# Optimization experiments

Hardware: AMD Instinct MI355X
Metric: run time of the kernel (lower is better)

## Reference

```python
import jax, jax.numpy as jnp
import numpy as np

NUM_STEPS = 5  # DVF2DDF(num_steps=5)


def _warp(vol, ddf, mode):
    """MONAI Warp: sample vol at (voxel index + ddf), align_corners=True, zeros padding.
    vol: [N,C,D,H,W]; ddf: [N,3,D,H,W] (channels = d,h,w displacement)."""
    N, C, D, H, W = vol.shape
    gd, gh, gw = jnp.meshgrid(jnp.arange(D, dtype=ddf.dtype),
                              jnp.arange(H, dtype=ddf.dtype),
                              jnp.arange(W, dtype=ddf.dtype), indexing='ij')
    cd = gd + ddf[:, 0]  # [N,D,H,W] absolute sample coords
    ch = gh + ddf[:, 1]
    cw = gw + ddf[:, 2]
    vol_flat = vol.reshape(N, C, D * H * W)

    def gather(di, hi, wi, valid):
        dc = jnp.clip(di, 0, D - 1)
        hc = jnp.clip(hi, 0, H - 1)
        wc = jnp.clip(wi, 0, W - 1)
        flat = ((dc * H + hc) * W + wc).reshape(N, 1, -1)
        v = jnp.take_along_axis(vol_flat, flat, axis=2).reshape(N, C, D, H, W)
        return v * valid[:, None]

    def in_bounds(di, hi, wi):
        return ((di >= 0) & (di < D) & (hi >= 0) & (hi < H)
                & (wi >= 0) & (wi < W)).astype(vol.dtype)

    if mode == 'nearest':
        di = jnp.round(cd).astype(jnp.int32)
        hi = jnp.round(ch).astype(jnp.int32)
        wi = jnp.round(cw).astype(jnp.int32)
        return gather(di, hi, wi, in_bounds(di, hi, wi))

    # trilinear ('bilinear' in grid_sample naming)
    d0 = jnp.floor(cd); h0 = jnp.floor(ch); w0 = jnp.floor(cw)
    fd = cd - d0; fh = ch - h0; fw = cw - w0
    d0i = d0.astype(jnp.int32); h0i = h0.astype(jnp.int32); w0i = w0.astype(jnp.int32)
    out = jnp.zeros_like(vol)
    for dd in (0, 1):
        for dh in (0, 1):
            for dw in (0, 1):
                di = d0i + dd; hi = h0i + dh; wi = w0i + dw
                wgt = ((fd if dd else 1 - fd)
                       * (fh if dh else 1 - fh)
                       * (fw if dw else 1 - fw))
                out = out + gather(di, hi, wi, in_bounds(di, hi, wi)) * wgt[:, None]
    return out


def _dvf2ddf(dvf, num_steps=NUM_STEPS):
    """Scaling-and-squaring integration of a stationary velocity field (MONAI DVF2DDF)."""
    ddf = dvf / (2 ** num_steps)
    for _ in range(num_steps):
        ddf = ddf + _warp(ddf, ddf, 'bilinear')
    return ddf


def setup_inputs() -> dict:
    key = jax.random.key(0)
    ks = jax.random.split(key, 6)
    D = H = W = 160
    return {
        "dvf0": jax.random.normal(ks[0], (1, 3, D, H, W), jnp.float32),
        "dvf1": jax.random.normal(ks[1], (1, 3, D, H, W), jnp.float32),
        "image": jax.random.normal(ks[2], (1, 1, D, H, W), jnp.float32),
        "cavity": jax.random.randint(ks[3], (1, 1, D, H, W), 0, 5, jnp.int32),
        "coronary": jax.random.randint(ks[4], (1, 1, D, H, W), 0, 3, jnp.int32),
        "w": jax.random.uniform(ks[5], (), jnp.float32),
    }


def reference(dvf0, dvf1, image, cavity, coronary, w):
    # linear blend of the two neighbouring phase DVFs
    dvf = dvf0 * (1 - w) + dvf1 * w
    ddf = _dvf2ddf(dvf)
    img_warped = _warp(image, ddf, 'bilinear')
    # labels are concatenated along batch and warped with nearest, ddf repeated
    labels = jnp.concatenate([cavity, coronary], axis=0).astype(jnp.float32)  # [2,1,D,H,W]
    lab_warped = _warp(labels, jnp.tile(ddf, (2, 1, 1, 1, 1)), 'nearest')
    cav_warped = lab_warped[0][None].astype(jnp.uint8)
    cor_warped = lab_warped[1][None].astype(jnp.uint8)
    return img_warped, cav_warped, cor_warped, ddf
```

## Files before the change

### kernel.cpp

```cpp
#include <hip/hip_runtime.h>

#define DD 160
#define HH 160
#define WW 160
#define PL (HH*WW)
#define S (DD*PL)

__device__ __forceinline__ float fmul(float a, float b){ return __fmul_rn(a,b); }
__device__ __forceinline__ float fadd(float a, float b){ return __fadd_rn(a,b); }
__device__ __forceinline__ float fsub(float a, float b){ return __fsub_rn(a,b); }


template<int H>
__global__ __launch_bounds__(256) void warp_step(const float* __restrict__ in,
                                                 float* __restrict__ out) {
    constexpr int RX = 32 + 2 * H;
    constexpr int RY = 8 + 2 * H;
    constexpr int RZ = 4 + 2 * H;
    constexpr int CH = RX * RY * RZ;
    __shared__ float smem[3 * CH];

    int b  = (blockIdx.x & 7) * 500 + (blockIdx.x >> 3);
    int ix = b % 5;
    int r  = b / 5;
    int iy = r % 20;
    int iz = r / 20;
    int x0 = ix << 5, y0 = iy << 3, z0 = iz << 2;
    int xs = x0 - H, ys = y0 - H, zs = z0 - H;

    int tid = threadIdx.x;
    for (int s = tid; s < CH; s += 256) {
        int rz  = s / (RY * RX);
        int rem = s - rz * (RY * RX);
        int ry  = rem / RX;
        int rx  = rem - ry * RX;
        int cz = min(max(zs + rz, 0), DD - 1);
        int cy = min(max(ys + ry, 0), HH - 1);
        int cx = min(max(xs + rx, 0), WW - 1);
        int q = (cz * HH + cy) * WW + cx;
        smem[s]          = in[q];
        smem[CH + s]     = in[S + q];
        smem[2 * CH + s] = in[2 * S + q];
    }
    __syncthreads();

    int lane = tid & 63, wid = tid >> 6;
    int x = x0 | (lane & 31);
    int y = y0 | (wid << 1) | (lane >> 5);

    for (int j = 0; j < 4; ++j) {
        int z = z0 + j;
        int p = (z * HH + y) * WW + x;
        int lc = ((j + H) * RY + (y - ys)) * RX + (x - xs);
        float vd = smem[lc], vh = smem[CH + lc], vw = smem[2 * CH + lc];

        float cd = fadd((float)z, vd);
        float ch = fadd((float)y, vh);
        float cw = fadd((float)x, vw);

        float d0 = floorf(cd), h0 = floorf(ch), w0 = floorf(cw);
        float fd = fsub(cd, d0), fh = fsub(ch, h0), fw = fsub(cw, w0);
        float gd = fsub(1.0f, fd), gh = fsub(1.0f, fh), gw = fsub(1.0f, fw);
        int d0i = (int)d0, h0i = (int)h0, w0i = (int)w0;

        int rd = d0i - zs, rh = h0i - ys, rw = w0i - xs;
        bool ok = ((unsigned)rd < (unsigned)(RZ - 1))
                & ((unsigned)rh < (unsigned)(RY - 1))
                & ((unsigned)rw < (unsigned)(RX - 1));

        float r0, r1, r2;
        if (ok) {
            bool vA0 = (d0i >= 0), vA1 = (d0i + 1 < DD);
            bool vB0 = (h0i >= 0), vB1 = (h0i + 1 < HH);
            bool vC0 = (w0i >= 0), vC1 = (w0i + 1 < WW);
            float wt[8];
            #pragma unroll
            for (int t = 0; t < 8; ++t) {
                int dd = t >> 2, dh = (t >> 1) & 1, dw = t & 1;
                bool valid = (dd ? vA1 : vA0) & (dh ? vB1 : vB0) & (dw ? vC1 : vC0);
                float wgt = fmul(fmul(dd ? fd : gd, dh ? fh : gh), dw ? fw : gw);
                wt[t] = valid ? wgt : 0.0f;
            }
            int l0 = (rd * RY + rh) * RX + rw;
            const int off[8] = { 0, 1, RX, RX + 1,
                                 RY * RX, RY * RX + 1, (RY + 1) * RX, (RY + 1) * RX + 1 };
            float acc0 = 0.0f, acc1 = 0.0f, acc2 = 0.0f;
            #pragma unroll
            for (int t = 0; t < 8; ++t) {
                int li = l0 + off[t];
                acc0 = fadd(acc0, fmul(smem[li], wt[t]));
                acc1 = fadd(acc1, fmul(smem[CH + li], wt[t]));
                acc2 = fadd(acc2, fmul(smem[2 * CH + li], wt[t]));
            }
            r0 = fadd(vd, acc0);
            r1 = fadd(vh, acc1);
            r2 = fadd(vw, acc2);
        } else {
            int   qa[8];
            float wt[8];
            #pragma unroll
            for (int t = 0; t < 8; ++t) {
                int dd = t >> 2, dh = (t >> 1) & 1, dw = t & 1;
                int di = d0i + dd, hi = h0i + dh, wi = w0i + dw;
                bool valid = (di >= 0) & (di < DD) & (hi >= 0) & (hi < HH)
                           & (wi >= 0) & (wi < WW);
                float wgt = fmul(fmul(dd ? fd : gd, dh ? fh : gh), dw ? fw : gw);
                wt[t] = valid ? wgt : 0.0f;
                int dc = min(max(di, 0), DD - 1);
                int hc = min(max(hi, 0), HH - 1);
                int wc = min(max(wi, 0), WW - 1);
                qa[t] = (dc * HH + hc) * WW + wc;
            }
            float acc0 = 0.0f, acc1 = 0.0f, acc2 = 0.0f;
            #pragma unroll
            for (int t = 0; t < 8; ++t) {
                acc0 = fadd(acc0, fmul(in[qa[t]], wt[t]));
                acc1 = fadd(acc1, fmul(in[S + qa[t]], wt[t]));
                acc2 = fadd(acc2, fmul(in[2 * S + qa[t]], wt[t]));
            }
            r0 = fadd(vd, acc0);
            r1 = fadd(vh, acc1);
            r2 = fadd(vw, acc2);
        }

        out[p] = r0; out[S + p] = r1; out[2 * S + p] = r2;
    }
}

__global__ __launch_bounds__(256) void fused_init_s1(const float* __restrict__ dvf0,
                                                     const float* __restrict__ dvf1,
                                                     const float* __restrict__ wp,
                                                     float* __restrict__ out) {
    constexpr int H = 1, RX = 34, RY = 10, RZ = 6, CH = RX * RY * RZ;
    __shared__ float smem[3 * CH];
    float w = wp[0];
    float onew = fsub(1.0f, w);

    int b  = (blockIdx.x & 7) * 500 + (blockIdx.x >> 3);
    int ix = b % 5;
    int r  = b / 5;
    int iy = r % 20;
    int iz = r / 20;
    int x0 = ix << 5, y0 = iy << 3, z0 = iz << 2;
    int xs = x0 - H, ys = y0 - H, zs = z0 - H;

    int tid = threadIdx.x;
    for (int s = tid; s < CH; s += 256) {
        int rz  = s / (RY * RX);
        int rem = s - rz * (RY * RX);
        int ry  = rem / RX;
        int rx  = rem - ry * RX;
        int cz = min(max(zs + rz, 0), DD - 1);
        int cy = min(max(ys + ry, 0), HH - 1);
        int cx = min(max(xs + rx, 0), WW - 1);
        int q = (cz * HH + cy) * WW + cx;
        #pragma unroll
        for (int c = 0; c < 3; ++c) {
            float a = dvf0[(size_t)c * S + q];
            float bb = dvf1[(size_t)c * S + q];
            smem[c * CH + s] = fmul(fadd(fmul(a, onew), fmul(bb, w)), 0.03125f);
        }
    }
    __syncthreads();

    int lane = tid & 63, wid = tid >> 6;
    int x = x0 | (lane & 31);
    int y = y0 | (wid << 1) | (lane >> 5);

    for (int j = 0; j < 4; ++j) {
        int z = z0 + j;
        int p = (z * HH + y) * WW + x;
        int lc = ((j + H) * RY + (y - ys)) * RX + (x - xs);
        float vd = smem[lc], vh = smem[CH + lc], vw = smem[2 * CH + lc];

        float cd = fadd((float)z, vd);
        float ch = fadd((float)y, vh);
        float cw = fadd((float)x, vw);

        float d0 = floorf(cd), h0 = floorf(ch), w0 = floorf(cw);
        float fd = fsub(cd, d0), fh = fsub(ch, h0), fw = fsub(cw, w0);
        float gd = fsub(1.0f, fd), gh = fsub(1.0f, fh), gw = fsub(1.0f, fw);
        int d0i = (int)d0, h0i = (int)h0, w0i = (int)w0;

        int rd = d0i - zs, rh = h0i - ys, rw = w0i - xs;
        bool ok = ((unsigned)rd < (unsigned)(RZ - 1))
                & ((unsigned)rh < (unsigned)(RY - 1))
                & ((unsigned)rw < (unsigned)(RX - 1));

        float r0, r1, r2;
        if (ok) {
            bool vA0 = (d0i >= 0), vA1 = (d0i + 1 < DD);
            bool vB0 = (h0i >= 0), vB1 = (h0i + 1 < HH);
            bool vC0 = (w0i >= 0), vC1 = (w0i + 1 < WW);
            float wt[8];
            #pragma unroll
            for (int t = 0; t < 8; ++t) {
                int dd = t >> 2, dh = (t >> 1) & 1, dw = t & 1;
                bool valid = (dd ? vA1 : vA0) & (dh ? vB1 : vB0) & (dw ? vC1 : vC0);
                float wgt = fmul(fmul(dd ? fd : gd, dh ? fh : gh), dw ? fw : gw);
                wt[t] = valid ? wgt : 0.0f;
            }
            int l0 = (rd * RY + rh) * RX + rw;
            const int off[8] = { 0, 1, RX, RX + 1,
                                 RY * RX, RY * RX + 1, (RY + 1) * RX, (RY + 1) * RX + 1 };
            float acc0 = 0.0f, acc1 = 0.0f, acc2 = 0.0f;
            #pragma unroll
            for (int t = 0; t < 8; ++t) {
                int li = l0 + off[t];
                acc0 = fadd(acc0, fmul(smem[li], wt[t]));
                acc1 = fadd(acc1, fmul(smem[CH + li], wt[t]));
                acc2 = fadd(acc2, fmul(smem[2 * CH + li], wt[t]));
            }
            r0 = fadd(vd, acc0);
            r1 = fadd(vh, acc1);
            r2 = fadd(vw, acc2);
        } else {
            int   qa[8];
            float wt[8];
            #pragma unroll
            for (int t = 0; t < 8; ++t) {
                int dd = t >> 2, dh = (t >> 1) & 1, dw = t & 1;
                int di = d0i + dd, hi = h0i + dh, wi = w0i + dw;
                bool valid = (di >= 0) & (di < DD) & (hi >= 0) & (hi < HH)
                           & (wi >= 0) & (wi < WW);
                float wgt = fmul(fmul(dd ? fd : gd, dh ? fh : gh), dw ? fw : gw);
                wt[t] = valid ? wgt : 0.0f;
                int dc = min(max(di, 0), DD - 1);
                int hc = min(max(hi, 0), HH - 1);
                int wc = min(max(wi, 0), WW - 1);
                qa[t] = (dc * HH + hc) * WW + wc;
            }
            float acc0 = 0.0f, acc1 = 0.0f, acc2 = 0.0f;
            #pragma unroll
            for (int t = 0; t < 8; ++t) {
                float ga = fmul(fadd(fmul(dvf0[qa[t]], onew), fmul(dvf1[qa[t]], w)), 0.03125f);
                float gb = fmul(fadd(fmul(dvf0[S + qa[t]], onew), fmul(dvf1[S + qa[t]], w)), 0.03125f);
                float gc = fmul(fadd(fmul(dvf0[2 * S + qa[t]], onew), fmul(dvf1[2 * S + qa[t]], w)), 0.03125f);
                acc0 = fadd(acc0, fmul(ga, wt[t]));
                acc1 = fadd(acc1, fmul(gb, wt[t]));
                acc2 = fadd(acc2, fmul(gc, wt[t]));
            }
            r0 = fadd(vd, acc0);
            r1 = fadd(vh, acc1);
            r2 = fadd(vw, acc2);
        }

        out[p] = r0; out[S + p] = r1; out[2 * S + p] = r2;
    }
}

__global__ __launch_bounds__(256) void final_fused(const float* __restrict__ ddf4,
                                                   const float* __restrict__ image,
                                                   const int* __restrict__ cav,
                                                   const int* __restrict__ cor,
                                                   float* __restrict__ outImg,
                                                   float* __restrict__ outDdf) {
    int b  = (blockIdx.x & 7) * 1000 + (blockIdx.x >> 3);
    int ix = b % 5;
    int r  = b / 5;
    int iy = r % 20;
    int iz = r / 20;
    int lane = threadIdx.x & 63, wid = threadIdx.x >> 6;
    int x  = (ix << 5) | (lane & 31);
    int y  = (iy << 3) | (wid << 1) | (lane >> 5);
    int z0 = iz << 1;
    int p0 = (z0 * HH + y) * WW + x;

    #pragma unroll
    for (int j = 0; j < 2; ++j) {
        int z = z0 + j;
        int p = p0 + j * PL;

        float vd = ddf4[p], vh = ddf4[S + p], vw = ddf4[2 * S + p];
        float cd = fadd((float)z, vd);
        float ch = fadd((float)y, vh);
        float cw = fadd((float)x, vw);

        float d0 = floorf(cd), h0 = floorf(ch), w0 = floorf(cw);
        float fd = fsub(cd, d0), fh = fsub(ch, h0), fw = fsub(cw, w0);
        float gd = fsub(1.0f, fd), gh = fsub(1.0f, fh), gw = fsub(1.0f, fw);
        int d0i = (int)d0, h0i = (int)h0, w0i = (int)w0;

        int   qa[8];
        float wt[8];
        #pragma unroll
        for (int t = 0; t < 8; ++t) {
            int dd = t >> 2, dh = (t >> 1) & 1, dw = t & 1;
            int di = d0i + dd, hi = h0i + dh, wi = w0i + dw;
            bool valid = (di >= 0) & (di < DD) & (hi >= 0) & (hi < HH)
                       & (wi >= 0) & (wi < WW);
            float wgt = fmul(fmul(dd ? fd : gd, dh ? fh : gh), dw ? fw : gw);
            wt[t] = valid ? wgt : 0.0f;
            int dc = min(max(di, 0), DD - 1);
            int hc = min(max(hi, 0), HH - 1);
            int wc = min(max(wi, 0), WW - 1);
            qa[t] = (dc * HH + hc) * WW + wc;
        }
        float acc0 = 0.0f, acc1 = 0.0f, acc2 = 0.0f;
        #pragma unroll
        for (int t = 0; t < 8; ++t) {
            acc0 = fadd(acc0, fmul(ddf4[qa[t]], wt[t]));
            acc1 = fadd(acc1, fmul(ddf4[S + qa[t]], wt[t]));
            acc2 = fadd(acc2, fmul(ddf4[2 * S + qa[t]], wt[t]));
        }
        float r0 = fadd(vd, acc0);
        float r1 = fadd(vh, acc1);
        float r2 = fadd(vw, acc2);
        outDdf[p] = r0; outDdf[S + p] = r1; outDdf[2 * S + p] = r2;

        float cd2 = fadd((float)z, r0);
        float ch2 = fadd((float)y, r1);
        float cw2 = fadd((float)x, r2);

        float d02 = floorf(cd2), h02 = floorf(ch2), w02 = floorf(cw2);
        float fd2 = fsub(cd2, d02), fh2 = fsub(ch2, h02), fw2 = fsub(cw2, w02);
        float gd2 = fsub(1.0f, fd2), gh2 = fsub(1.0f, fh2), gw2 = fsub(1.0f, fw2);
        int d2i = (int)d02, h2i = (int)h02, w2i = (int)w02;

        bool fast = ((unsigned)d2i < (unsigned)(DD - 1))
                  & ((unsigned)h2i < (unsigned)(HH - 1))
                  & ((unsigned)w2i < (unsigned)(WW - 1));
        if (fast) {
            const float* bp0 = image + (d2i * HH + h2i) * WW + w2i;
            const float* bp1 = bp0 + PL;
            float g[8];
            g[0] = bp0[0];      g[1] = bp0[1];
            g[2] = bp0[WW];     g[3] = bp0[WW + 1];
            g[4] = bp1[0];      g[5] = bp1[1];
            g[6] = bp1[WW];     g[7] = bp1[WW + 1];
            float w00 = fmul(gd2, gh2), w01 = fmul(gd2, fh2);
            float w10 = fmul(fd2, gh2), w11 = fmul(fd2, fh2);
            float wtf[8] = { fmul(w00, gw2), fmul(w00, fw2), fmul(w01, gw2), fmul(w01, fw2),
                             fmul(w10, gw2), fmul(w10, fw2), fmul(w11, gw2), fmul(w11, fw2) };
            float acc = 0.0f;
            #pragma unroll
            for (int t = 0; t < 8; ++t) acc = fadd(acc, fmul(g[t], wtf[t]));
            outImg[p] = acc;

            int di = (int)rintf(cd2), hi = (int)rintf(ch2), wi = (int)rintf(cw2);
            int q = (di * HH + hi) * WW + wi;
            outImg[S + p]     = (float)cav[q];
            outImg[2 * S + p] = (float)cor[q];
        } else {
            int   qb[8];
            float wtf[8];
            #pragma unroll
            for (int t = 0; t < 8; ++t) {
                int dd = t >> 2, dh = (t >> 1) & 1, dw = t & 1;
                int di = d2i + dd, hi = h2i + dh, wi = w2i + dw;
                bool valid = (di >= 0) & (di < DD) & (hi >= 0) & (hi < HH)
                           & (wi >= 0) & (wi < WW);
                float wgt = fmul(fmul(dd ? fd2 : gd2, dh ? fh2 : gh2), dw ? fw2 : gw2);
                wtf[t] = valid ? wgt : 0.0f;
                int dc = min(max(di, 0), DD - 1);
                int hc = min(max(hi, 0), HH - 1);
                int wc = min(max(wi, 0), WW - 1);
                qb[t] = (dc * HH + hc) * WW + wc;
            }
            float acc = 0.0f;
            #pragma unroll
            for (int t = 0; t < 8; ++t) acc = fadd(acc, fmul(image[qb[t]], wtf[t]));
            outImg[p] = acc;

            int di = (int)rintf(cd2), hi = (int)rintf(ch2), wi = (int)rintf(cw2);
            bool valid = (di >= 0) & (di < DD) & (hi >= 0) & (hi < HH)
                       & (wi >= 0) & (wi < WW);
            int dc = min(max(di, 0), DD - 1);
            int hc = min(max(hi, 0), HH - 1);
            int wc = min(max(wi, 0), WW - 1);
            int q = (dc * HH + hc) * WW + wc;
            outImg[S + p]     = valid ? (float)cav[q] : 0.0f;
            outImg[2 * S + p] = valid ? (float)cor[q] : 0.0f;
        }
    }
}

__global__ __launch_bounds__(256) void warp_flat(const float* __restrict__ in,
                                                 float* __restrict__ out) {
    int b  = (blockIdx.x & 7) * 1000 + (blockIdx.x >> 3);
    int ix = b % 5;
    int r  = b / 5;
    int iy = r % 20;
    int iz = r / 20;
    int lane = threadIdx.x & 63, wid = threadIdx.x >> 6;
    int x  = (ix << 5) | (lane & 31);
    int y  = (iy << 3) | (wid << 1) | (lane >> 5);
    int z0 = iz << 1;
    int p0 = (z0 * HH + y) * WW + x;

    #pragma unroll
    for (int j = 0; j < 2; ++j) {
        int z = z0 + j;
        int p = p0 + j * PL;
        float vd = in[p], vh = in[S + p], vw = in[2 * S + p];
        float cd = fadd((float)z, vd);
        float ch = fadd((float)y, vh);
        float cw = fadd((float)x, vw);

        float d0 = floorf(cd), h0 = floorf(ch), w0 = floorf(cw);
        float fd = fsub(cd, d0), fh = fsub(ch, h0), fw = fsub(cw, w0);
        float gd = fsub(1.0f, fd), gh = fsub(1.0f, fh), gw = fsub(1.0f, fw);
        int d0i = (int)d0, h0i = (int)h0, w0i = (int)w0;

        int   qa[8];
        float wt[8];
        #pragma unroll
        for (int t = 0; t < 8; ++t) {
            int dd = t >> 2, dh = (t >> 1) & 1, dw = t & 1;
            int di = d0i + dd, hi = h0i + dh, wi = w0i + dw;
            bool valid = (di >= 0) & (di < DD) & (hi >= 0) & (hi < HH)
                       & (wi >= 0) & (wi < WW);
            float wgt = fmul(fmul(dd ? fd : gd, dh ? fh : gh), dw ? fw : gw);
            wt[t] = valid ? wgt : 0.0f;
            int dc = min(max(di, 0), DD - 1);
            int hc = min(max(hi, 0), HH - 1);
            int wc = min(max(wi, 0), WW - 1);
            qa[t] = (dc * HH + hc) * WW + wc;
        }
        float acc0 = 0.0f, acc1 = 0.0f, acc2 = 0.0f;
        #pragma unroll
        for (int t = 0; t < 8; ++t) {
            acc0 = fadd(acc0, fmul(in[qa[t]], wt[t]));
            acc1 = fadd(acc1, fmul(in[S + qa[t]], wt[t]));
            acc2 = fadd(acc2, fmul(in[2 * S + qa[t]], wt[t]));
        }
        out[p]         = fadd(vd, acc0);
        out[S + p]     = fadd(vh, acc1);
        out[2 * S + p] = fadd(vw, acc2);
    }
}

__global__ __launch_bounds__(256) void final_kernel(const float* __restrict__ ddf,
                                                    const float* __restrict__ image,
                                                    const int* __restrict__ cav,
                                                    const int* __restrict__ cor,
                                                    float* __restrict__ out) {
    int b  = (blockIdx.x & 7) * 1000 + (blockIdx.x >> 3);
    int ix = b % 5;
    int r  = b / 5;
    int iy = r % 20;
    int iz = r / 20;
    int lane = threadIdx.x & 63, wid = threadIdx.x >> 6;
    int x  = (ix << 5) | (lane & 31);
    int y  = (iy << 3) | (wid << 1) | (lane >> 5);
    int z0 = iz << 1;
    int p0 = (z0 * HH + y) * WW + x;

    #pragma unroll
    for (int j = 0; j < 2; ++j) {
        int z = z0 + j;
        int p = p0 + j * PL;
        float cd = fadd((float)z, ddf[p]);
        float ch = fadd((float)y, ddf[S + p]);
        float cw = fadd((float)x, ddf[2 * S + p]);

        float d0 = floorf(cd), h0 = floorf(ch), w0 = floorf(cw);
        float fd = fsub(cd, d0), fh = fsub(ch, h0), fw = fsub(cw, w0);
        float gd = fsub(1.0f, fd), gh = fsub(1.0f, fh), gw = fsub(1.0f, fw);
        int d0i = (int)d0, h0i = (int)h0, w0i = (int)w0;

        int   qa[8];
        float wt[8];
        #pragma unroll
        for (int t = 0; t < 8; ++t) {
            int dd = t >> 2, dh = (t >> 1) & 1, dw = t & 1;
            int di = d0i + dd, hi = h0i + dh, wi = w0i + dw;
            bool valid = (di >= 0) & (di < DD) & (hi >= 0) & (hi < HH)
                       & (wi >= 0) & (wi < WW);
            float wgt = fmul(fmul(dd ? fd : gd, dh ? fh : gh), dw ? fw : gw);
            wt[t] = valid ? wgt : 0.0f;
            int dc = min(max(di, 0), DD - 1);
            int hc = min(max(hi, 0), HH - 1);
            int wc = min(max(wi, 0), WW - 1);
            qa[t] = (dc * HH + hc) * WW + wc;
        }
        float acc = 0.0f;
        #pragma unroll
        for (int t = 0; t < 8; ++t) acc = fadd(acc, fmul(image[qa[t]], wt[t]));
        out[p] = acc;

        int di = (int)rintf(cd), hi = (int)rintf(ch), wi = (int)rintf(cw);
        bool valid = (di >= 0) & (di < DD) & (hi >= 0) & (hi < HH)
                   & (wi >= 0) & (wi < WW);
        int dc = min(max(di, 0), DD - 1);
        int hc = min(max(hi, 0), HH - 1);
        int wc = min(max(wi, 0), WW - 1);
        int q = (dc * HH + hc) * WW + wc;
        out[S + p]     = valid ? (float)cav[q] : 0.0f;
        out[2 * S + p] = valid ? (float)cor[q] : 0.0f;
    }
}

extern "C" void kernel_launch(void* const* d_in, const int* in_sizes, int n_in,
                              void* d_out, int out_size, void* d_ws, size_t ws_size,
                              hipStream_t stream) {
    const float* dvf0   = (const float*)d_in[0];
    const float* dvf1   = (const float*)d_in[1];
    const float* image  = (const float*)d_in[2];
    const int*   cav    = (const int*)d_in[3];
    const int*   cor    = (const int*)d_in[4];
    const float* w      = (const float*)d_in[5];

    float* out  = (float*)d_out;
    float* bufA = out;
    float* bufB = out + (size_t)3 * S;
    float* bufC = (float*)d_ws;
    bool useWs = (d_ws != nullptr) && (ws_size >= (size_t)3 * S * sizeof(float));

    fused_init_s1<<<4000, 256, 0, stream>>>(dvf0, dvf1, w, bufB);
    warp_step<1><<<4000, 256, 0, stream>>>(bufB, bufA);
    warp_step<1><<<4000, 256, 0, stream>>>(bufA, bufB);
    if (useWs) {
        warp_step<2><<<4000, 256, 0, stream>>>(bufB, bufC);
        final_fused<<<8000, 256, 0, stream>>>(bufC, image, cav, cor, bufA, bufB);
    } else {
        warp_step<2><<<4000, 256, 0, stream>>>(bufB, bufA);
        warp_flat<<<8000, 256, 0, stream>>>(bufA, bufB);
        final_kernel<<<8000, 256, 0, stream>>>(bufB, image, cav, cor, bufA);
    }
}
```

Before: 414.1 us.

## Vectorize halo loads with float4 and tile final step through phased shared memory

The halo tile loads in warp_step and fused_init_s1 now use float4 global reads into a 40-wide padded row layout in place of scalar per-element loads with a 3D index decode. The final fused kernel is replaced by a version that caches a 4x8x32 tile with a 3-voxel halo in shared memory, loading one displacement channel at a time to keep LDS small. It precomputes weights for four z-slices before accumulating from shared memory. Voxels whose samples fall outside the halo still gather from global memory. Costs are a wider halo with redundant loads, extra barriers per channel, and higher register pressure from holding weights for four slices.

```diff
diff --git a/kernel.cpp b/kernel.cpp
--- a/kernel.cpp
+++ b/kernel.cpp
@@ -14,11 +14,12 @@
 template<int H>
 __global__ __launch_bounds__(256) void warp_step(const float* __restrict__ in,
                                                  float* __restrict__ out) {
-    constexpr int RX = 32 + 2 * H;
+    constexpr int RZ = 4 + 2 * H;
     constexpr int RY = 8 + 2 * H;
-    constexpr int RZ = 4 + 2 * H;
-    constexpr int CH = RX * RY * RZ;
-    __shared__ float smem[3 * CH];
+    constexpr int ROWS = RZ * RY;
+    constexpr int NCH4 = ROWS * 10;
+    constexpr int CHF  = ROWS * 40;
+    __shared__ float smem[3 * CHF];
 
     int b  = (blockIdx.x & 7) * 500 + (blockIdx.x >> 3);
     int ix = b % 5;
@@ -26,33 +27,37 @@
     int iy = r % 20;
     int iz = r / 20;
     int x0 = ix << 5, y0 = iy << 3, z0 = iz << 2;
-    int xs = x0 - H, ys = y0 - H, zs = z0 - H;
+    int xs4 = x0 - 4, ys = y0 - H, zs = z0 - H;
 
     int tid = threadIdx.x;
-    for (int s = tid; s < CH; s += 256) {
-        int rz  = s / (RY * RX);
-        int rem = s - rz * (RY * RX);
-        int ry  = rem / RX;
-        int rx  = rem - ry * RX;
+    for (int c = tid; c < NCH4; c += 256) {
+        int row = c / 10;
+        int col = (c - row * 10) << 2;
+        int rz  = row / RY;
+        int ry  = row - rz * RY;
         int cz = min(max(zs + rz, 0), DD - 1);
         int cy = min(max(ys + ry, 0), HH - 1);
-        int cx = min(max(xs + rx, 0), WW - 1);
-        int q = (cz * HH + cy) * WW + cx;
-        smem[s]          = in[q];
-        smem[CH + s]     = in[S + q];
-        smem[2 * CH + s] = in[2 * S + q];
+        int q  = min(max((cz * HH + cy) * WW + xs4 + col, 0), S - 4);
+        float4 v0 = *(const float4*)(in + q);
+        float4 v1 = *(const float4*)(in + S + q);
+        float4 v2 = *(const float4*)(in + 2 * S + q);
+        *(float4*)&smem[row * 40 + col]           = v0;
+        *(float4*)&smem[CHF + row * 40 + col]     = v1;
+        *(float4*)&smem[2 * CHF + row * 40 + col] = v2;
     }
     __syncthreads();
 
     int lane = tid & 63, wid = tid >> 6;
     int x = x0 | (lane & 31);
     int y = y0 | (wid << 1) | (lane >> 5);
+    int lx = x - xs4;
+    int ly = y - ys;
 
     for (int j = 0; j < 4; ++j) {
         int z = z0 + j;
         int p = (z * HH + y) * WW + x;
-        int lc = ((j + H) * RY + (y - ys)) * RX + (x - xs);
-        float vd = smem[lc], vh = smem[CH + lc], vw = smem[2 * CH + lc];
+        int lc = ((j + H) * RY + ly) * 40 + lx;
+        float vd = smem[lc], vh = smem[CHF + lc], vw = smem[2 * CHF + lc];
 
         float cd = fadd((float)z, vd);
         float ch = fadd((float)y, vh);
@@ -63,10 +68,10 @@
         float gd = fsub(1.0f, fd), gh = fsub(1.0f, fh), gw = fsub(1.0f, fw);
         int d0i = (int)d0, h0i = (int)h0, w0i = (int)w0;
 
-        int rd = d0i - zs, rh = h0i - ys, rw = w0i - xs;
+        int rd = d0i - zs, rh = h0i - ys, rw = w0i - xs4;
         bool ok = ((unsigned)rd < (unsigned)(RZ - 1))
                 & ((unsigned)rh < (unsigned)(RY - 1))
-                & ((unsigned)rw < (unsigned)(RX - 1));
+                & ((unsigned)rw < 39u);
 
         float r0, r1, r2;
         if (ok) {
@@ -81,16 +86,16 @@
                 float wgt = fmul(fmul(dd ? fd : gd, dh ? fh : gh), dw ? fw : gw);
                 wt[t] = valid ? wgt : 0.0f;
             }
-            int l0 = (rd * RY + rh) * RX + rw;
-            const int off[8] = { 0, 1, RX, RX + 1,
-                                 RY * RX, RY * RX + 1, (RY + 1) * RX, (RY + 1) * RX + 1 };
+            int l0 = (rd * RY + rh) * 40 + rw;
+            const int off[8] = { 0, 1, 40, 41,
+                                 RY * 40, RY * 40 + 1, (RY + 1) * 40, (RY + 1) * 40 + 1 };
             float acc0 = 0.0f, acc1 = 0.0f, acc2 = 0.0f;
             #pragma unroll
             for (int t = 0; t < 8; ++t) {
                 int li = l0 + off[t];
                 acc0 = fadd(acc0, fmul(smem[li], wt[t]));
-                acc1 = fadd(acc1, fmul(smem[CH + li], wt[t]));
-                acc2 = fadd(acc2, fmul(smem[2 * CH + li], wt[t]));
+                acc1 = fadd(acc1, fmul(smem[CHF + li], wt[t]));
+                acc2 = fadd(acc2, fmul(smem[2 * CHF + li], wt[t]));
             }
             r0 = fadd(vd, acc0);
             r1 = fadd(vh, acc1);
@@ -131,8 +136,8 @@
                                                      const float* __restrict__ dvf1,
                                                      const float* __restrict__ wp,
                                                      float* __restrict__ out) {
-    constexpr int H = 1, RX = 34, RY = 10, RZ = 6, CH = RX * RY * RZ;
-    __shared__ float smem[3 * CH];
+    constexpr int H = 1, RZ = 6, RY = 10, ROWS = 60, NCH4 = 600, CHF = 2400;
+    __shared__ float smem[3 * CHF];
     float w = wp[0];
     float onew = fsub(1.0f, w);
 
@@ -142,23 +147,26 @@
     int iy = r % 20;
     int iz = r / 20;
     int x0 = ix << 5, y0 = iy << 3, z0 = iz << 2;
-    int xs = x0 - H, ys = y0 - H, zs = z0 - H;
+    int xs4 = x0 - 4, ys = y0 - H, zs = z0 - H;
 
     int tid = threadIdx.x;
-    for (int s = tid; s < CH; s += 256) {
-        int rz  = s / (RY * RX);
-        int rem = s - rz * (RY * RX);
-        int ry  = rem / RX;
-        int rx  = rem - ry * RX;
+    for (int c = tid; c < NCH4; c += 256) {
+        int row = c / 10;
+        int col = (c - row * 10) << 2;
+        int rz  = row / RY;
+        int ry  = row - rz * RY;
         int cz = min(max(zs + rz, 0), DD - 1);
         int cy = min(max(ys + ry, 0), HH - 1);
-        int cx = min(max(xs + rx, 0), WW - 1);
-        int q = (cz * HH + cy) * WW + cx;
+        int q  = min(max((cz * HH + cy) * WW + xs4 + col, 0), S - 4);
         #pragma unroll
-        for (int c = 0; c < 3; ++c) {
-            float a = dvf0[(size_t)c * S + q];
-            float bb = dvf1[(size_t)c * S + q];
-            smem[c * CH + s] = fmul(fadd(fmul(a, onew), fmul(bb, w)), 0.03125f);
+        for (int ch = 0; ch < 3; ++ch) {
+            float A[4], B[4], O[4];
+            *(float4*)A = *(const float4*)(dvf0 + (size_t)ch * S + q);
+            *(float4*)B = *(const float4*)(dvf1 + (size_t)ch * S + q);
+            #pragma unroll
+            for (int k = 0; k < 4; ++k)
+                O[k] = fmul(fadd(fmul(A[k], onew), fmul(B[k], w)), 0.03125f);
+            *(float4*)&smem[ch * CHF + row * 40 + col] = *(float4*)O;
         }
     }
     __syncthreads();
@@ -166,12 +174,14 @@
     int lane = tid & 63, wid = tid >> 6;
     int x = x0 | (lane & 31);
     int y = y0 | (wid << 1) | (lane >> 5);
+    int lx = x - xs4;
+    int ly = y - ys;
 
     for (int j = 0; j < 4; ++j) {
         int z = z0 + j;
         int p = (z * HH + y) * WW + x;
-        int lc = ((j + H) * RY + (y - ys)) * RX + (x - xs);
-        float vd = smem[lc], vh = smem[CH + lc], vw = smem[2 * CH + lc];
+        int lc = ((j + H) * RY + ly) * 40 + lx;
+        float vd = smem[lc], vh = smem[CHF + lc], vw = smem[2 * CHF + lc];
 
         float cd = fadd((float)z, vd);
         float ch = fadd((float)y, vh);
@@ -182,10 +192,10 @@
         float gd = fsub(1.0f, fd), gh = fsub(1.0f, fh), gw = fsub(1.0f, fw);
         int d0i = (int)d0, h0i = (int)h0, w0i = (int)w0;
 
-        int rd = d0i - zs, rh = h0i - ys, rw = w0i - xs;
+        int rd = d0i - zs, rh = h0i - ys, rw = w0i - xs4;
         bool ok = ((unsigned)rd < (unsigned)(RZ - 1))
                 & ((unsigned)rh < (unsigned)(RY - 1))
-                & ((unsigned)rw < (unsigned)(RX - 1));
+                & ((unsigned)rw < 39u);
 
         float r0, r1, r2;
         if (ok) {
@@ -200,16 +210,16 @@
                 float wgt = fmul(fmul(dd ? fd : gd, dh ? fh : gh), dw ? fw : gw);
                 wt[t] = valid ? wgt : 0.0f;
             }
-            int l0 = (rd * RY + rh) * RX + rw;
-            const int off[8] = { 0, 1, RX, RX + 1,
-                                 RY * RX, RY * RX + 1, (RY + 1) * RX, (RY + 1) * RX + 1 };
+            int l0 = (rd * RY + rh) * 40 + rw;
+            const int off[8] = { 0, 1, 40, 41,
+                                 RY * 40, RY * 40 + 1, (RY + 1) * 40, (RY + 1) * 40 + 1 };
             float acc0 = 0.0f, acc1 = 0.0f, acc2 = 0.0f;
             #pragma unroll
             for (int t = 0; t < 8; ++t) {
                 int li = l0 + off[t];
                 acc0 = fadd(acc0, fmul(smem[li], wt[t]));
-                acc1 = fadd(acc1, fmul(smem[CH + li], wt[t]));
-                acc2 = fadd(acc2, fmul(smem[2 * CH + li], wt[t]));
+                acc1 = fadd(acc1, fmul(smem[CHF + li], wt[t]));
+                acc2 = fadd(acc2, fmul(smem[2 * CHF + li], wt[t]));
             }
             r0 = fadd(vd, acc0);
             r1 = fadd(vh, acc1);
@@ -249,69 +259,145 @@
     }
 }
 
-__global__ __launch_bounds__(256) void final_fused(const float* __restrict__ ddf4,
-                                                   const float* __restrict__ image,
-                                                   const int* __restrict__ cav,
-                                                   const int* __restrict__ cor,
-                                                   float* __restrict__ outImg,
-                                                   float* __restrict__ outDdf) {
-    int b  = (blockIdx.x & 7) * 1000 + (blockIdx.x >> 3);
+__global__ __launch_bounds__(256) void final_phased(const float* __restrict__ ddf4,
+                                                    const float* __restrict__ image,
+                                                    const int* __restrict__ cav,
+                                                    const int* __restrict__ cor,
+                                                    float* __restrict__ outImg,
+                                                    float* __restrict__ outDdf) {
+    constexpr int RZ = 10, RY = 14, ROWS = 140, NCH4 = 1400, CHF = 5600;
+    __shared__ float smem[CHF];
+
+    int b  = (blockIdx.x & 7) * 500 + (blockIdx.x >> 3);
     int ix = b % 5;
     int r  = b / 5;
     int iy = r % 20;
     int iz = r / 20;
-    int lane = threadIdx.x & 63, wid = threadIdx.x >> 6;
-    int x  = (ix << 5) | (lane & 31);
-    int y  = (iy << 3) | (wid << 1) | (lane >> 5);
-    int z0 = iz << 1;
+    int x0 = ix << 5, y0 = iy << 3, z0 = iz << 2;
+    int xs4 = x0 - 4, ys = y0 - 3, zs = z0 - 3;
+
+    int tid = threadIdx.x;
+    int lane = tid & 63, wid = tid >> 6;
+    int x = x0 | (lane & 31);
+    int y = y0 | (wid << 1) | (lane >> 5);
     int p0 = (z0 * HH + y) * WW + x;
 
+    float ctd[4], cth[4], ctw[4];
     #pragma unroll
-    for (int j = 0; j < 2; ++j) {
+    for (int j = 0; j < 4; ++j) {
+        ctd[j] = ddf4[p0 + j * PL];
+        cth[j] = ddf4[S + p0 + j * PL];
+        ctw[j] = ddf4[2 * S + p0 + j * PL];
+    }
+
+    float wt[4][8];
+    int   l0[4];
+    int   okm = 0;
+    const int off[8] = { 0, 1, 40, 41,
+                         RY * 40, RY * 40 + 1, (RY + 1) * 40, (RY + 1) * 40 + 1 };
+    #pragma unroll
+    for (int j = 0; j < 4; ++j) {
         int z = z0 + j;
-        int p = p0 + j * PL;
-
-        float vd = ddf4[p], vh = ddf4[S + p], vw = ddf4[2 * S + p];
-        float cd = fadd((float)z, vd);
-        float ch = fadd((float)y, vh);
-        float cw = fadd((float)x, vw);
-
+        float cd = fadd((float)z, ctd[j]);
+        float ch = fadd((float)y, cth[j]);
+        float cw = fadd((float)x, ctw[j]);
         float d0 = floorf(cd), h0 = floorf(ch), w0 = floorf(cw);
         float fd = fsub(cd, d0), fh = fsub(ch, h0), fw = fsub(cw, w0);
         float gd = fsub(1.0f, fd), gh = fsub(1.0f, fh), gw = fsub(1.0f, fw);
         int d0i = (int)d0, h0i = (int)h0, w0i = (int)w0;
 
-        int   qa[8];
-        float wt[8];
+        bool vA0 = (d0i >= 0), vA1 = (d0i + 1 < DD);
+        bool vB0 = (h0i >= 0), vB1 = (h0i + 1 < HH);
+        bool vC0 = (w0i >= 0), vC1 = (w0i + 1 < WW);
         #pragma unroll
         for (int t = 0; t < 8; ++t) {
             int dd = t >> 2, dh = (t >> 1) & 1, dw = t & 1;
-            int di = d0i + dd, hi = h0i + dh, wi = w0i + dw;
-            bool valid = (di >= 0) & (di < DD) & (hi >= 0) & (hi < HH)
-                       & (wi >= 0) & (wi < WW);
+            bool valid = (dd ? vA1 : vA0) & (dh ? vB1 : vB0) & (dw ? vC1 : vC0);
             float wgt = fmul(fmul(dd ? fd : gd, dh ? fh : gh), dw ? fw : gw);
-            wt[t] = valid ? wgt : 0.0f;
-            int dc = min(max(di, 0), DD - 1);
-            int hc = min(max(hi, 0), HH - 1);
-            int wc = min(max(wi, 0), WW - 1);
-            qa[t] = (dc * HH + hc) * WW + wc;
-        }
-        float acc0 = 0.0f, acc1 = 0.0f, acc2 = 0.0f;
+            wt[j][t] = valid ? wgt : 0.0f;
+        }
+        int rd = d0i - zs, rh = h0i - ys, rw = w0i - xs4;
+        bool ok = ((unsigned)rd < (unsigned)(RZ - 1))
+                & ((unsigned)rh < (unsigned)(RY - 1))
+                & ((unsigned)rw < 39u);
+        l0[j] = (rd * RY + rh) * 40 + rw;
+        okm |= (ok ? 1 : 0) << j;
+    }
+
+    float acc[3][4] = {{0,0,0,0},{0,0,0,0},{0,0,0,0}};
+    #pragma unroll
+    for (int c = 0; c < 3; ++c) {
+        if (c) __syncthreads();
+        const float* src = ddf4 + (size_t)c * S;
+        for (int cc = tid; cc < NCH4; cc += 256) {
+            int row = cc / 10;
+            int col = (cc - row * 10) << 2;
+            int rz  = row / RY;
+            int ry  = row - rz * RY;
+            int cz = min(max(zs + rz, 0), DD - 1);
+            int cy = min(max(ys + ry, 0), HH - 1);
+            int q  = min(max((cz * HH + cy) * WW + xs4 + col, 0), S - 4);
+            *(float4*)&smem[row * 40 + col] = *(const float4*)(src + q);
+        }
+        __syncthreads();
         #pragma unroll
-        for (int t = 0; t < 8; ++t) {
-            acc0 = fadd(acc0, fmul(ddf4[qa[t]], wt[t]));
-            acc1 = fadd(acc1, fmul(ddf4[S + qa[t]], wt[t]));
-            acc2 = fadd(acc2, fmul(ddf4[2 * S + qa[t]], wt[t]));
-        }
-        float r0 = fadd(vd, acc0);
-        float r1 = fadd(vh, acc1);
-        float r2 = fadd(vw, acc2);
+        for (int j = 0; j < 4; ++j) {
+            if ((okm >> j) & 1) {
+                #pragma unroll
+                for (int t = 0; t < 8; ++t)
+                    acc[c][j] = fadd(acc[c][j], fmul(smem[l0[j] + off[t]], wt[j][t]));
+            }
+        }
+    }
+
+    #pragma unroll
+    for (int j = 0; j < 4; ++j) {
+        int z = z0 + j;
+        int p = p0 + j * PL;
+        float r0, r1, r2;
+        if ((okm >> j) & 1) {
+            r0 = fadd(ctd[j], acc[0][j]);
+            r1 = fadd(cth[j], acc[1][j]);
+            r2 = fadd(ctw[j], acc[2][j]);
+        } else {
+            float cd = fadd((float)z, ctd[j]);
+            float ch = fadd((float)y, cth[j]);
+            float cw = fadd((float)x, ctw[j]);
+            float d0 = floorf(cd), h0 = floorf(ch), w0 = floorf(cw);
+            float fd = fsub(cd, d0), fh = fsub(ch, h0), fw = fsub(cw, w0);
+            float gd = fsub(1.0f, fd), gh = fsub(1.0f, fh), gw = fsub(1.0f, fw);
+            int d0i = (int)d0, h0i = (int)h0, w0i = (int)w0;
+            int   qa[8];
+            float wtf[8];
+            #pragma unroll
+            for (int t = 0; t < 8; ++t) {
+                int dd = t >> 2, dh = (t >> 1) & 1, dw = t & 1;
+                int di = d0i + dd, hi = h0i + dh, wi = w0i + dw;
+                bool valid = (di >= 0) & (di < DD) & (hi >= 0) & (hi < HH)
+                           & (wi >= 0) & (wi < WW);
+                float wgt = fmul(fmul(dd ? fd : gd, dh ? fh : gh), dw ? fw : gw);
+                wtf[t] = valid ? wgt : 0.0f;
+                int dc = min(max(di, 0), DD - 1);
+                int hc = min(max(hi, 0), HH - 1);
+                int wc = min(max(wi, 0), WW - 1);
+                qa[t] = (dc * HH + hc) * WW + wc;
+            }
+            float a0 = 0.0f, a1 = 0.0f, a2 = 0.0f;
+            #pragma unroll
+            for (int t = 0; t < 8; ++t) {
+                a0 = fadd(a0, fmul(ddf4[qa[t]], wtf[t]));
+                a1 = fadd(a1, fmul(ddf4[S + qa[t]], wtf[t]));
+                a2 = fadd(a2, fmul(ddf4[2 * S + qa[t]], wtf[t]));
+            }
+            r0 = fadd(ctd[j], a0);
+            r1 = fadd(cth[j], a1);
+            r2 = fadd(ctw[j], a2);
+        }
         outDdf[p] = r0; outDdf[S + p] = r1; outDdf[2 * S + p] = r2;
 
         float cd2 = fadd((float)z, r0);
         float ch2 = fadd((float)y, r1);
         float cw2 = fadd((float)x, r2);
-
         float d02 = floorf(cd2), h02 = floorf(ch2), w02 = floorf(cw2);
         float fd2 = fsub(cd2, d02), fh2 = fsub(ch2, h02), fw2 = fsub(cw2, w02);
         float gd2 = fsub(1.0f, fd2), gh2 = fsub(1.0f, fh2), gw2 = fsub(1.0f, fw2);
@@ -332,10 +418,10 @@
             float w10 = fmul(fd2, gh2), w11 = fmul(fd2, fh2);
             float wtf[8] = { fmul(w00, gw2), fmul(w00, fw2), fmul(w01, gw2), fmul(w01, fw2),
                              fmul(w10, gw2), fmul(w10, fw2), fmul(w11, gw2), fmul(w11, fw2) };
-            float acc = 0.0f;
-            #pragma unroll
-            for (int t = 0; t < 8; ++t) acc = fadd(acc, fmul(g[t], wtf[t]));
-            outImg[p] = acc;
+            float a = 0.0f;
+            #pragma unroll
+            for (int t = 0; t < 8; ++t) a = fadd(a, fmul(g[t], wtf[t]));
+            outImg[p] = a;
 
             int di = (int)rintf(cd2), hi = (int)rintf(ch2), wi = (int)rintf(cw2);
             int q = (di * HH + hi) * WW + wi;
@@ -357,10 +443,10 @@
                 int wc = min(max(wi, 0), WW - 1);
                 qb[t] = (dc * HH + hc) * WW + wc;
             }
-            float acc = 0.0f;
-            #pragma unroll
-            for (int t = 0; t < 8; ++t) acc = fadd(acc, fmul(image[qb[t]], wtf[t]));
-            outImg[p] = acc;
+            float a = 0.0f;
+            #pragma unroll
+            for (int t = 0; t < 8; ++t) a = fadd(a, fmul(image[qb[t]], wtf[t]));
+            outImg[p] = a;
 
             int di = (int)rintf(cd2), hi = (int)rintf(ch2), wi = (int)rintf(cw2);
             bool valid = (di >= 0) & (di < DD) & (hi >= 0) & (hi < HH)
@@ -512,7 +598,7 @@
     warp_step<1><<<4000, 256, 0, stream>>>(bufA, bufB);
     if (useWs) {
         warp_step<2><<<4000, 256, 0, stream>>>(bufB, bufC);
-        final_fused<<<8000, 256, 0, stream>>>(bufC, image, cav, cor, bufA, bufB);
+        final_phased<<<4000, 256, 0, stream>>>(bufC, image, cav, cor, bufA, bufB);
     } else {
         warp_step<2><<<4000, 256, 0, stream>>>(bufB, bufA);
         warp_flat<<<8000, 256, 0, stream>>>(bufA, bufB);
```

Result: faster. 376.8 us (-9.0%).
